# Performance work log

Measured on AMD Instinct MI355X. Metric: run time of the kernel, lower is better.

The kernel has to match this reference:

```python
import jax, jax.numpy as jnp
import numpy as np

B, T, D, H = 512, 128, 384, 6
DH = D // H  # 64
DFF = 4 * D  # 1536
EPS = 1e-5


def layer_norm(x, g, b):
    mu = jnp.mean(x, axis=-1, keepdims=True)
    var = jnp.var(x, axis=-1, keepdims=True)
    return (x - mu) * jax.lax.rsqrt(var + EPS) * g + b


def setup_inputs() -> dict:
    key = jax.random.key(0)
    ks = jax.random.split(key, 12)
    s = lambda *sh: 1.0 / np.sqrt(sh[0])
    return {
        "x": jax.random.normal(ks[0], (B, T, D), dtype=jnp.float32),
        "Wq": jax.random.normal(ks[1], (D, D), dtype=jnp.float32) * s(D),
        "Wk": jax.random.normal(ks[2], (D, D), dtype=jnp.float32) * s(D),
        "Wv": jax.random.normal(ks[3], (D, D), dtype=jnp.float32) * s(D),
        "Wo": jax.random.normal(ks[4], (D, D), dtype=jnp.float32) * s(D),
        "bo": jnp.zeros((D,), jnp.float32),
        "W1": jax.random.normal(ks[5], (D, DFF), dtype=jnp.float32) * s(D),
        "b1": jnp.zeros((DFF,), jnp.float32),
        "W2": jax.random.normal(ks[6], (DFF, D), dtype=jnp.float32) * s(DFF),
        "b2": jnp.zeros((D,), jnp.float32),
        "g1": jnp.ones((D,), jnp.float32),
        "be1": jnp.zeros((D,), jnp.float32),
        "g2": jnp.ones((D,), jnp.float32),
        "be2": jnp.zeros((D,), jnp.float32),
    }


def reference(x, Wq, Wk, Wv, Wo, bo, W1, b1, W2, b2, g1, be1, g2, be2):
    # --- multi-head causal self-attention on layer_norm1(x) ---
    h = layer_norm(x, g1, be1)
    q = (h @ Wq).reshape(B, T, H, DH)
    k = (h @ Wk).reshape(B, T, H, DH)
    v = (h @ Wv).reshape(B, T, H, DH)
    scores = jnp.einsum("bthd,bshd->bhts", q, k) * (DH ** -0.5)  # [B,H,T,T]
    causal = jnp.tril(jnp.ones((T, T), dtype=bool))
    scores = jnp.where(causal, scores, -jnp.inf)
    attn = jax.nn.softmax(scores, axis=-1)
    o = jnp.einsum("bhts,bshd->bthd", attn, v).reshape(B, T, D)
    x = x + o @ Wo + bo
    # --- feed-forward on layer_norm2(x) ---
    h2 = layer_norm(x, g2, be2)
    ff = jax.nn.relu(h2 @ W1 + b1) @ W2 + b2
    return x + ff
```

## Files before the change

kernel.cpp:

```cpp
#include <hip/hip_runtime.h>

#define B_   512
#define T_   128
#define D_   384
#define H_   6
#define DH_  64
#define DFF_ 1536
#define NROW (B_*T_)

typedef __attribute__((ext_vector_type(8))) short bf16x8;
typedef __attribute__((ext_vector_type(4))) float f32x4;

__device__ __forceinline__ unsigned short f2bf(float f) {
  union { float f; unsigned u; } v; v.f = f;
  unsigned r = v.u + 0x7fffu + ((v.u >> 16) & 1u);
  return (unsigned short)(r >> 16);
}

#define GLDS16(gp, lp)                                                     \
  __builtin_amdgcn_global_load_lds(                                        \
      (const __attribute__((address_space(1))) void*)(gp),                 \
      (__attribute__((address_space(3))) void*)(lp), 16, 0, 0)

#define BAR_LGKM() asm volatile("s_waitcnt lgkmcnt(0)\n\ts_barrier" ::: "memory")

__global__ void wt_kernel(const float* __restrict__ W, unsigned short* __restrict__ WT,
                          int K, int Nn) {
  int id = blockIdx.x * 256 + threadIdx.x;
  if (id >= K * Nn) return;
  int n = id % Nn, kk = id / Nn;
  WT[(size_t)n * K + kk] = f2bf(W[(size_t)kk * Nn + n]);
}

__global__ void pack_w1(const unsigned short* __restrict__ W1T,
                        unsigned short* __restrict__ W1P) {
  int tid = blockIdx.x * 256 + threadIdx.x;
  int lane = tid & 63, frag = tid >> 6;
  int k = frag % 12, t2 = frag / 12;
  int mi = t2 & 1, t3 = t2 >> 1;
  int w = t3 & 3, c = t3 >> 2;
  int l15 = lane & 15, lq = lane >> 4;
  int r = c * 128 + w * 32 + mi * 16 + l15;
  int col = k * 32 + lq * 8;
  *(int4*)(W1P + (size_t)tid * 8) = *(const int4*)(W1T + (size_t)r * 384 + col);
}
__global__ void pack_w2(const unsigned short* __restrict__ W2T,
                        unsigned short* __restrict__ W2P) {
  int tid = blockIdx.x * 256 + threadIdx.x;
  int lane = tid & 63, frag = tid >> 6;
  int kk = frag & 3, t2 = frag >> 2;
  int c = t2 % 12, t3 = t2 / 12;
  int mi = t3 % 6, w = t3 / 6;
  int l15 = lane & 15, lq = lane >> 4;
  int r = w * 96 + mi * 16 + l15;
  int col = c * 128 + kk * 32 + lq * 8;
  *(int4*)(W2P + (size_t)tid * 8) = *(const int4*)(W2T + (size_t)r * 1536 + col);
}

__global__ __launch_bounds__(256) void ln_kernel(const float* __restrict__ x,
                                                 const float* __restrict__ g,
                                                 const float* __restrict__ be,
                                                 unsigned short* __restrict__ out) {
  int row = (blockIdx.x * 256 + threadIdx.x) >> 6;
  int l = threadIdx.x & 63;
  const float* xr = x + (size_t)row * D_;
  float v[6]; float s = 0.f, ss = 0.f;
  #pragma unroll
  for (int i = 0; i < 6; ++i) { v[i] = xr[l + i*64]; s += v[i]; ss += v[i]*v[i]; }
  #pragma unroll
  for (int m = 1; m < 64; m <<= 1) { s += __shfl_xor(s, m); ss += __shfl_xor(ss, m); }
  float mu  = s * (1.f / D_);
  float var = ss * (1.f / D_) - mu * mu;
  float rs  = rsqrtf(var + 1e-5f);
  unsigned short* orow = out + (size_t)row * D_;
  #pragma unroll
  for (int i = 0; i < 6; ++i) {
    int c = l + i*64;
    orow[c] = f2bf((v[i] - mu) * rs * g[c] + be[c]);
  }
}

template<int EPI>
__global__ __launch_bounds__(256) void gemm_bt(const unsigned short* __restrict__ A,
                                               const unsigned short* __restrict__ BT,
                                               void* __restrict__ Cc,
                                               const float* __restrict__ bias,
                                               const float* __restrict__ res,
                                               int Nn, int K) {
  __shared__ unsigned short As[2][128][32];
  __shared__ unsigned short Bs[2][128][32];
  int tid = threadIdx.x, w = tid >> 6, l = tid & 63;
  int wr = w >> 1, wc = w & 1;

  int ncol = gridDim.y;
  int nwg  = gridDim.x * ncol;
  int lin  = blockIdx.y * gridDim.x + blockIdx.x;
  int cpx  = nwg >> 3;
  int swz  = (lin & 7) * cpx + (lin >> 3);
  size_t R0 = (size_t)(swz / ncol) * 128;
  int C0 = (swz % ncol) * 128;

  int seg0 = (w * 2 + 0) * 16;
  int seg1 = (w * 2 + 1) * 16;
  int srow0 = seg0 + (l >> 2);
  int srow1 = seg1 + (l >> 2);
  int scol  = (l & 3) * 8;

  const unsigned short* ga0 = A  + (R0 + srow0) * K + scol;
  const unsigned short* ga1 = A  + (R0 + srow1) * K + scol;
  const unsigned short* gb0 = BT + (size_t)(C0 + srow0) * K + scol;
  const unsigned short* gb1 = BT + (size_t)(C0 + srow1) * K + scol;

  f32x4 acc[4][4];
  #pragma unroll
  for (int i = 0; i < 4; ++i)
    #pragma unroll
    for (int j = 0; j < 4; ++j) acc[i][j] = (f32x4){0.f, 0.f, 0.f, 0.f};

  GLDS16(ga0, &As[0][seg0][0]);
  GLDS16(ga1, &As[0][seg1][0]);
  GLDS16(gb0, &Bs[0][seg0][0]);
  GLDS16(gb1, &Bs[0][seg1][0]);
  ga0 += 32; ga1 += 32; gb0 += 32; gb1 += 32;

  int nk = K >> 5;
  for (int t = 0; t < nk; ++t) {
    int cur = t & 1;
    __syncthreads();
    if (t + 1 < nk) {
      GLDS16(ga0, &As[cur ^ 1][seg0][0]);
      GLDS16(ga1, &As[cur ^ 1][seg1][0]);
      GLDS16(gb0, &Bs[cur ^ 1][seg0][0]);
      GLDS16(gb1, &Bs[cur ^ 1][seg1][0]);
      ga0 += 32; ga1 += 32; gb0 += 32; gb1 += 32;
    }
    bf16x8 af[4], bf[4];
    #pragma unroll
    for (int mi = 0; mi < 4; ++mi)
      af[mi] = *(const bf16x8*)(&As[cur][wr*64 + mi*16 + (l & 15)][(l >> 4) * 8]);
    #pragma unroll
    for (int ni = 0; ni < 4; ++ni)
      bf[ni] = *(const bf16x8*)(&Bs[cur][wc*64 + ni*16 + (l & 15)][(l >> 4) * 8]);
    #pragma unroll
    for (int mi = 0; mi < 4; ++mi)
      #pragma unroll
      for (int ni = 0; ni < 4; ++ni)
        acc[mi][ni] = __builtin_amdgcn_mfma_f32_16x16x32_bf16(af[mi], bf[ni], acc[mi][ni], 0, 0, 0);
  }

  #pragma unroll
  for (int mi = 0; mi < 4; ++mi) {
    #pragma unroll
    for (int ni = 0; ni < 4; ++ni) {
      int col = C0 + wc*64 + ni*16 + (l & 15);
      #pragma unroll
      for (int j = 0; j < 4; ++j) {
        size_t row = R0 + wr*64 + mi*16 + ((l >> 4) << 2) + j;
        float vv = acc[mi][ni][j];
        if (EPI == 1) {
          ((float*)Cc)[row * Nn + col] = vv + bias[col] + res[row * Nn + col];
        } else {
          int buf = col / 384, c2 = col - buf * 384;
          ((unsigned short*)Cc)[(size_t)buf * NROW * 384 + row * 384 + c2] = f2bf(vv);
        }
      }
    }
  }
}

#define LDA3(dst, pA, k0)                                                    \
  { _Pragma("unroll") for (int kq = 0; kq < 3; ++kq)                         \
      dst[kq] = *(const bf16x8*)((pA) + ((k0) + kq) * 512); }

#define CMP3(buf, k0, acc)                                                   \
  { _Pragma("unroll") for (int kq = 0; kq < 3; ++kq) {                       \
      bf16x8 bfr[4];                                                         \
      _Pragma("unroll") for (int ni = 0; ni < 4; ++ni)                       \
        bfr[ni] = *(const bf16x8*)(smem + (ni*12 + (k0)+kq)*1024 + l*16);    \
      _Pragma("unroll") for (int ni = 0; ni < 4; ++ni)                       \
        acc[ni] = __builtin_amdgcn_mfma_f32_16x16x32_bf16(                   \
            buf[kq], bfr[ni], acc[ni], 0, 0, 0);                             \
    } }

__global__ __launch_bounds__(512, 4) void ffn_fused(
    const unsigned short* __restrict__ h2,
    const unsigned short* __restrict__ w1P,
    const unsigned short* __restrict__ w2P,
    const float* __restrict__ b1,
    const float* __restrict__ b2,
    float* __restrict__ out)
{
  __shared__ __align__(16) char smem[65536];
  int tid = threadIdx.x, w = tid >> 6, l = tid & 63;
  int l15 = l & 15, lq = l >> 4;
  size_t R0 = (size_t)blockIdx.x * 64;

  {
    int row = tid >> 3, gi = row >> 4, l15w = row & 15;
    int cbase = (tid & 7) * 48;
    const unsigned short* src = h2 + (R0 + row) * 384 + cbase;
    #pragma unroll
    for (int i = 0; i < 6; ++i) {
      int col = cbase + i * 8;
      int k = col >> 5, lqw = (col >> 3) & 3;
      *(int4*)(smem + (gi*12 + k)*1024 + (lqw*16 + l15w)*16) = *(const int4*)(src + i*8);
    }
  }
  __syncthreads();

  f32x4 oacc[3][4];
  #pragma unroll
  for (int i = 0; i < 3; ++i)
    #pragma unroll
    for (int j = 0; j < 4; ++j) oacc[i][j] = (f32x4){0.f, 0.f, 0.f, 0.f};

  const unsigned short* w1b = w1P + w * 6144  + l * 8;
  const unsigned short* w2b = w2P + w * 73728 + l * 8;

  #define LDV(dst, pV, kk)                                                   \
    { _Pragma("unroll") for (int mi = 0; mi < 3; ++mi)                       \
        dst[mi] = *(const bf16x8*)((pV) + mi * 24576 + (kk) * 512); }

  #define CMPV(buf, kk)                                                      \
    { bf16x8 bv[4];                                                          \
      _Pragma("unroll") for (int ni = 0; ni < 4; ++ni)                       \
        bv[ni] = *(const bf16x8*)(smem + 49152 + (ni*4 + (kk))*1024 + l*16); \
      _Pragma("unroll") for (int mi = 0; mi < 3; ++mi)                       \
        _Pragma("unroll") for (int ni = 0; ni < 4; ++ni)                     \
          oacc[mi][ni] = __builtin_amdgcn_mfma_f32_16x16x32_bf16(            \
              buf[mi], bv[ni], oacc[mi][ni], 0, 0, 0);                       \
    }

  bf16x8 afA[3], afB[3];
  bf16x8 avA[3], avB[3];

  LDA3(afA, w1b, 0)

  for (int c = 0; c < 12; ++c) {
    const unsigned short* pA = w1b + (size_t)c * 49152;
    const unsigned short* pV = w2b + c * 2048;

    f32x4 pacc[4];
    #pragma unroll
    for (int j = 0; j < 4; ++j) pacc[j] = (f32x4){0.f, 0.f, 0.f, 0.f};

    LDA3(afB, pA, 3)
    __builtin_amdgcn_s_setprio(1); CMP3(afA, 0, pacc) __builtin_amdgcn_s_setprio(0);
    LDA3(afA, pA, 6)
    __builtin_amdgcn_s_setprio(1); CMP3(afB, 3, pacc) __builtin_amdgcn_s_setprio(0);
    LDA3(afB, pA, 9)
    __builtin_amdgcn_s_setprio(1); CMP3(afA, 6, pacc) __builtin_amdgcn_s_setprio(0);
    LDV(avA, pV, 0)
    __builtin_amdgcn_s_setprio(1); CMP3(afB, 9, pacc) __builtin_amdgcn_s_setprio(0);

    {
      int fcb = c * 128 + w * 16 + lq * 4;
      float4 bb = *(const float4*)(b1 + fcb);
      unsigned pw = (unsigned)(49152 + (w >> 1) * 1024 +
                    (((w & 1) * 2 + (lq >> 1)) * 16 + l15) * 16 + (lq & 1) * 8);
      #pragma unroll
      for (int ni = 0; ni < 4; ++ni) {
        float p0 = pacc[ni][0] + bb.x;
        float p1 = pacc[ni][1] + bb.y;
        float p2 = pacc[ni][2] + bb.z;
        float p3 = pacc[ni][3] + bb.w;
        ushort4 pk;
        pk.x = f2bf(p0 > 0.f ? p0 : 0.f);
        pk.y = f2bf(p1 > 0.f ? p1 : 0.f);
        pk.z = f2bf(p2 > 0.f ? p2 : 0.f);
        pk.w = f2bf(p3 > 0.f ? p3 : 0.f);
        *(ushort4*)(smem + pw + ni * 4096) = pk;
      }
    }
    BAR_LGKM();

    const unsigned short* pAn = w1b + (size_t)(c < 11 ? c + 1 : 11) * 49152;
    LDV(avB, pV, 1)
    __builtin_amdgcn_s_setprio(1); CMPV(avA, 0) __builtin_amdgcn_s_setprio(0);
    LDV(avA, pV, 2)
    __builtin_amdgcn_s_setprio(1); CMPV(avB, 1) __builtin_amdgcn_s_setprio(0);
    LDV(avB, pV, 3)
    __builtin_amdgcn_s_setprio(1); CMPV(avA, 2) __builtin_amdgcn_s_setprio(0);
    LDA3(afA, pAn, 0)
    __builtin_amdgcn_s_setprio(1); CMPV(avB, 3) __builtin_amdgcn_s_setprio(0);
    BAR_LGKM();
  }
  #undef LDV
  #undef CMPV

  #pragma unroll
  for (int mi = 0; mi < 3; ++mi) {
    int ocb = w * 48 + mi * 16 + lq * 4;
    float4 b2v = *(const float4*)(b2 + ocb);
    #pragma unroll
    for (int ni = 0; ni < 4; ++ni) {
      size_t row = R0 + ni * 16 + l15;
      float* op = out + row * D_ + ocb;
      float4 r = *(const float4*)op;
      float4 o;
      o.x = oacc[mi][ni][0] + b2v.x + r.x;
      o.y = oacc[mi][ni][1] + b2v.y + r.y;
      o.z = oacc[mi][ni][2] + b2v.z + r.z;
      o.w = oacc[mi][ni][3] + b2v.w + r.w;
      *(float4*)op = o;
    }
  }
}

__global__ __launch_bounds__(256) void attn_kernel(const unsigned short* __restrict__ q,
                                                   const unsigned short* __restrict__ k,
                                                   const unsigned short* __restrict__ v,
                                                   unsigned short* __restrict__ o) {
  __shared__ __align__(16) char smem[52224];
  unsigned short (*Ks)[72]       = (unsigned short(*)[72])smem;
  unsigned short (*Ps)[32][136]  = (unsigned short(*)[32][136])smem;
  unsigned short (*Vt)[136]      = (unsigned short(*)[136])(smem + 34816);

  int bh = blockIdx.x;
  int b = bh / H_, h = bh % H_;
  int tid = threadIdx.x, w = tid >> 6, l = tid & 63;

  const unsigned short* kb = k + ((size_t)b * T_) * D_ + h * DH_;
  const unsigned short* vb = v + ((size_t)b * T_) * D_ + h * DH_;
  #pragma unroll
  for (int it = 0; it < 4; ++it) {
    int id = it * 256 + tid;
    int s = id >> 3, c8 = (id & 7) * 8;
    int4 kv = *(const int4*)(kb + (size_t)s * D_ + c8);
    *(int4*)(&Ks[s][c8]) = kv;
    int4 vv = *(const int4*)(vb + (size_t)s * D_ + c8);
    const unsigned short* pe = (const unsigned short*)&vv;
    #pragma unroll
    for (int j2 = 0; j2 < 8; ++j2) Vt[c8 + j2][s] = pe[j2];
  }
  __syncthreads();

  const unsigned short* qbp = q + ((size_t)b * T_) * D_ + h * DH_;
  int rowbase = w * 32;
  bf16x8 aq[2][2];
  #pragma unroll
  for (int mi = 0; mi < 2; ++mi)
    #pragma unroll
    for (int ks = 0; ks < 2; ++ks)
      aq[mi][ks] = *(const bf16x8*)(qbp + (size_t)(rowbase + mi*16 + (l & 15)) * D_
                                        + ks*32 + ((l >> 4) << 3));

  f32x4 accs[2][8];
  #pragma unroll
  for (int i = 0; i < 2; ++i)
    #pragma unroll
    for (int j = 0; j < 8; ++j) accs[i][j] = (f32x4){0.f, 0.f, 0.f, 0.f};
  #pragma unroll
  for (int ks = 0; ks < 2; ++ks) {
    bf16x8 bk[8];
    #pragma unroll
    for (int ni = 0; ni < 8; ++ni)
      bk[ni] = *(const bf16x8*)(&Ks[ni*16 + (l & 15)][ks*32 + ((l >> 4) << 3)]);
    __builtin_amdgcn_s_setprio(1);
    #pragma unroll
    for (int mi = 0; mi < 2; ++mi)
      #pragma unroll
      for (int ni = 0; ni < 8; ++ni)
        accs[mi][ni] = __builtin_amdgcn_mfma_f32_16x16x32_bf16(aq[mi][ks], bk[ni], accs[mi][ni], 0, 0, 0);
    __builtin_amdgcn_s_setprio(0);
  }
  __syncthreads();

  #pragma unroll
  for (int mi = 0; mi < 2; ++mi) {
    #pragma unroll
    for (int j = 0; j < 4; ++j) {
      int t = rowbase + mi*16 + ((l >> 4) << 2) + j;
      float mx = -1e30f;
      #pragma unroll
      for (int ni = 0; ni < 8; ++ni) {
        int scol = ni*16 + (l & 15);
        float sv = accs[mi][ni][j] * 0.125f;
        sv = (scol <= t) ? sv : -1e30f;
        accs[mi][ni][j] = sv;
        mx = fmaxf(mx, sv);
      }
      mx = fmaxf(mx, __shfl_xor(mx, 1));
      mx = fmaxf(mx, __shfl_xor(mx, 2));
      mx = fmaxf(mx, __shfl_xor(mx, 4));
      mx = fmaxf(mx, __shfl_xor(mx, 8));
      float sum = 0.f;
      #pragma unroll
      for (int ni = 0; ni < 8; ++ni) {
        float e = __expf(accs[mi][ni][j] - mx);
        accs[mi][ni][j] = e;
        sum += e;
      }
      sum += __shfl_xor(sum, 1);
      sum += __shfl_xor(sum, 2);
      sum += __shfl_xor(sum, 4);
      sum += __shfl_xor(sum, 8);
      float inv = 1.f / sum;
      #pragma unroll
      for (int ni = 0; ni < 8; ++ni)
        Ps[w][mi*16 + ((l >> 4) << 2) + j][ni*16 + (l & 15)] = f2bf(accs[mi][ni][j] * inv);
    }
  }
  __syncthreads();

  f32x4 acco[2][4];
  #pragma unroll
  for (int i = 0; i < 2; ++i)
    #pragma unroll
    for (int j = 0; j < 4; ++j) acco[i][j] = (f32x4){0.f, 0.f, 0.f, 0.f};
  #pragma unroll
  for (int ks = 0; ks < 4; ++ks) {
    bf16x8 ap[2], bv[4];
    #pragma unroll
    for (int mi = 0; mi < 2; ++mi)
      ap[mi] = *(const bf16x8*)(&Ps[w][mi*16 + (l & 15)][ks*32 + ((l >> 4) << 3)]);
    #pragma unroll
    for (int ni = 0; ni < 4; ++ni)
      bv[ni] = *(const bf16x8*)(&Vt[ni*16 + (l & 15)][ks*32 + ((l >> 4) << 3)]);
    __builtin_amdgcn_s_setprio(1);
    #pragma unroll
    for (int mi = 0; mi < 2; ++mi)
      #pragma unroll
      for (int ni = 0; ni < 4; ++ni)
        acco[mi][ni] = __builtin_amdgcn_mfma_f32_16x16x32_bf16(ap[mi], bv[ni], acco[mi][ni], 0, 0, 0);
    __builtin_amdgcn_s_setprio(0);
  }

  unsigned short* ob = o + ((size_t)b * T_) * D_ + h * DH_;
  #pragma unroll
  for (int mi = 0; mi < 2; ++mi)
    #pragma unroll
    for (int ni = 0; ni < 4; ++ni)
      #pragma unroll
      for (int j = 0; j < 4; ++j) {
        int t = rowbase + mi*16 + ((l >> 4) << 2) + j;
        int d = ni*16 + (l & 15);
        ob[(size_t)t * D_ + d] = f2bf(acco[mi][ni][j]);
      }
}

extern "C" void kernel_launch(void* const* d_in, const int* in_sizes, int n_in,
                              void* d_out, int out_size, void* d_ws, size_t ws_size,
                              hipStream_t stream) {
  const float* x   = (const float*)d_in[0];
  const float* Wq  = (const float*)d_in[1];
  const float* Wk  = (const float*)d_in[2];
  const float* Wv  = (const float*)d_in[3];
  const float* Wo  = (const float*)d_in[4];
  const float* bo  = (const float*)d_in[5];
  const float* W1  = (const float*)d_in[6];
  const float* b1  = (const float*)d_in[7];
  const float* W2  = (const float*)d_in[8];
  const float* b2  = (const float*)d_in[9];
  const float* g1  = (const float*)d_in[10];
  const float* be1 = (const float*)d_in[11];
  const float* g2  = (const float*)d_in[12];
  const float* be2 = (const float*)d_in[13];

  char* ws = (char*)d_ws;
  unsigned short* hb   = (unsigned short*)(ws);
  unsigned short* qb   = (unsigned short*)(ws +  50331648);
  unsigned short* kbuf = (unsigned short*)(ws + 100663296);
  unsigned short* vbuf = (unsigned short*)(ws + 150994944);
  unsigned short* wqT  = (unsigned short*)(ws + 201326592);
  unsigned short* wkT  = wqT + 147456;
  unsigned short* wvT  = wkT + 147456;
  unsigned short* woT  = wvT + 147456;
  unsigned short* w1T  = woT + 147456;
  unsigned short* w2T  = w1T + 589824;
  unsigned short* w1P  = w2T + 589824;
  unsigned short* w2P  = w1P + 589824;
  float* x2 = (float*)d_out;
  (void)kbuf; (void)vbuf;

  wt_kernel<<<dim3(576),  256, 0, stream>>>(Wq, wqT, 384, 384);
  wt_kernel<<<dim3(576),  256, 0, stream>>>(Wk, wkT, 384, 384);
  wt_kernel<<<dim3(576),  256, 0, stream>>>(Wv, wvT, 384, 384);
  wt_kernel<<<dim3(576),  256, 0, stream>>>(Wo, woT, 384, 384);
  wt_kernel<<<dim3(2304), 256, 0, stream>>>(W1, w1T, 384, 1536);
  wt_kernel<<<dim3(2304), 256, 0, stream>>>(W2, w2T, 1536, 384);
  pack_w1<<<dim3(288), 256, 0, stream>>>(w1T, w1P);
  pack_w2<<<dim3(288), 256, 0, stream>>>(w2T, w2P);

  ln_kernel<<<dim3(NROW / 4), 256, 0, stream>>>(x, g1, be1, hb);

  gemm_bt<3><<<dim3(NROW / 128, 9), 256, 0, stream>>>(hb, wqT, qb, nullptr, nullptr, 1152, 384);

  attn_kernel<<<dim3(B_ * H_), 256, 0, stream>>>(qb, kbuf, vbuf, qb);

  gemm_bt<1><<<dim3(NROW / 128, 3), 256, 0, stream>>>(qb, woT, x2, bo, x, 384, 384);

  ln_kernel<<<dim3(NROW / 4), 256, 0, stream>>>((const float*)x2, g2, be2, hb);

  ffn_fused<<<dim3(NROW / 64), 512, 0, stream>>>(hb, w1P, w2P, b1, b2, x2);
}
```

Before: 447.1 us.

## Replace QKV projection GEMM with dedicated kernel streaming prepacked weights from global

Adds a specialized QKV GEMM kernel. Each 512-thread block stages a 32-row tile of the layernormed activations in LDS once, streams prepacked Wqkv fragments directly from global memory into registers with software prefetch and setprio around the MFMAs, and writes bf16 outputs through LDS as coalesced 16-byte stores. The Wq/Wk/Wv transposes are made contiguous and packed by the existing pack_w1 kernel, and the generic gemm_bt loses its bf16 scatter epilogue. This aims to remove the strided 2-byte scatter stores and the LDS staging of B tiles. In exchange every block re-reads the full weight matrix, which relies on cache hits, and each tile covers only 32 rows.

```diff
diff --git a/kernel.cpp b/kernel.cpp
--- a/kernel.cpp
+++ b/kernel.cpp
@@ -80,6 +80,95 @@
   }
 }
 
+__global__ __launch_bounds__(512, 4) void qkv_gemm(
+    const unsigned short* __restrict__ h, const unsigned short* __restrict__ wP,
+    unsigned short* __restrict__ qkv)
+{
+  __shared__ __align__(16) char smem[25600];
+  int tid = threadIdx.x, w = tid >> 6, l = tid & 63;
+  int l15 = l & 15, lq = l >> 4;
+  size_t R0 = (size_t)blockIdx.x * 32;
+
+  {
+    int row = tid >> 4, gi = row >> 4, l15w = row & 15;
+    const unsigned short* src = h + (R0 + row) * 384 + (tid & 15) * 24;
+    #pragma unroll
+    for (int i = 0; i < 3; ++i) {
+      int col = (tid & 15) * 24 + i * 8;
+      int k = col >> 5, lqw = (col >> 3) & 3;
+      *(int4*)(smem + (gi*12 + k)*1024 + (lqw*16 + l15w)*16) = *(const int4*)(src + i*8);
+    }
+  }
+  __syncthreads();
+
+  f32x4 acc[9][2];
+  #pragma unroll
+  for (int c = 0; c < 9; ++c)
+    #pragma unroll
+    for (int ni = 0; ni < 2; ++ni) acc[c][ni] = (f32x4){0.f, 0.f, 0.f, 0.f};
+
+  const unsigned short* wb = wP + l * 8;
+
+  #define LDG(dst, cb, k)                                                    \
+    { _Pragma("unroll") for (int ci = 0; ci < 3; ++ci)                       \
+        dst[ci] = *(const bf16x8*)(wb + (((cb)+ci)*8 + w) * 6144 + (k) * 512); }
+
+  #define CMPG(buf, cb)                                                      \
+    { _Pragma("unroll") for (int ci = 0; ci < 3; ++ci)                       \
+        _Pragma("unroll") for (int ni = 0; ni < 2; ++ni)                     \
+          acc[(cb)+ci][ni] = __builtin_amdgcn_mfma_f32_16x16x32_bf16(        \
+              buf[ci], bfr[ni], acc[(cb)+ci][ni], 0, 0, 0); }
+
+  bf16x8 a0[3], a1[3], a2[3];
+  LDG(a0, 0, 0)
+
+  for (int k = 0; k < 12; ++k) {
+    bf16x8 bfr[2];
+    #pragma unroll
+    for (int ni = 0; ni < 2; ++ni)
+      bfr[ni] = *(const bf16x8*)(smem + (ni*12 + k)*1024 + l*16);
+    int kn = (k < 11) ? k + 1 : 11;
+    LDG(a1, 3, k)
+    __builtin_amdgcn_s_setprio(1); CMPG(a0, 0) __builtin_amdgcn_s_setprio(0);
+    LDG(a2, 6, k)
+    __builtin_amdgcn_s_setprio(1); CMPG(a1, 3) __builtin_amdgcn_s_setprio(0);
+    LDG(a0, 0, kn)
+    __builtin_amdgcn_s_setprio(1); CMPG(a2, 6) __builtin_amdgcn_s_setprio(0);
+  }
+  #undef LDG
+  #undef CMPG
+
+  __syncthreads();
+  #pragma unroll
+  for (int buf = 0; buf < 3; ++buf) {
+    #pragma unroll
+    for (int ci = 0; ci < 3; ++ci) {
+      int c = buf * 3 + ci;
+      #pragma unroll
+      for (int ni = 0; ni < 2; ++ni) {
+        int row = ni * 16 + l15;
+        ushort4 pk;
+        pk.x = f2bf(acc[c][ni][0]);
+        pk.y = f2bf(acc[c][ni][1]);
+        pk.z = f2bf(acc[c][ni][2]);
+        pk.w = f2bf(acc[c][ni][3]);
+        *(ushort4*)(smem + row * 784 + ci * 256 + w * 32 + lq * 8) = pk;
+      }
+    }
+    __syncthreads();
+    {
+      int row = tid >> 4;
+      unsigned short* obase = qkv + (size_t)buf * NROW * 384 + (R0 + row) * 384;
+      #pragma unroll
+      for (int i = 0; i < 3; ++i) {
+        int ob = (tid & 15) * 16 + i * 256;
+        *(int4*)(obase + (ob >> 1)) = *(const int4*)(smem + row * 784 + ob);
+      }
+    }
+    __syncthreads();
+  }
+}
+
 template<int EPI>
 __global__ __launch_bounds__(256) void gemm_bt(const unsigned short* __restrict__ A,
                                                const unsigned short* __restrict__ BT,
@@ -157,12 +246,7 @@
       for (int j = 0; j < 4; ++j) {
         size_t row = R0 + wr*64 + mi*16 + ((l >> 4) << 2) + j;
         float vv = acc[mi][ni][j];
-        if (EPI == 1) {
-          ((float*)Cc)[row * Nn + col] = vv + bias[col] + res[row * Nn + col];
-        } else {
-          int buf = col / 384, c2 = col - buf * 384;
-          ((unsigned short*)Cc)[(size_t)buf * NROW * 384 + row * 384 + c2] = f2bf(vv);
-        }
+        ((float*)Cc)[row * Nn + col] = vv + bias[col] + res[row * Nn + col];
       }
     }
   }
@@ -458,33 +542,33 @@
   const float* be2 = (const float*)d_in[13];
 
   char* ws = (char*)d_ws;
-  unsigned short* hb   = (unsigned short*)(ws);
-  unsigned short* qb   = (unsigned short*)(ws +  50331648);
-  unsigned short* kbuf = (unsigned short*)(ws + 100663296);
-  unsigned short* vbuf = (unsigned short*)(ws + 150994944);
-  unsigned short* wqT  = (unsigned short*)(ws + 201326592);
-  unsigned short* wkT  = wqT + 147456;
-  unsigned short* wvT  = wkT + 147456;
-  unsigned short* woT  = wvT + 147456;
-  unsigned short* w1T  = woT + 147456;
-  unsigned short* w2T  = w1T + 589824;
-  unsigned short* w1P  = w2T + 589824;
-  unsigned short* w2P  = w1P + 589824;
+  unsigned short* hb    = (unsigned short*)(ws);
+  unsigned short* qb    = (unsigned short*)(ws +  50331648);
+  unsigned short* kbuf  = (unsigned short*)(ws + 100663296);
+  unsigned short* vbuf  = (unsigned short*)(ws + 150994944);
+  unsigned short* wqT   = (unsigned short*)(ws + 201326592);
+  unsigned short* woT   = wqT + 442368;
+  unsigned short* w1T   = woT + 147456;
+  unsigned short* w2T   = w1T + 589824;
+  unsigned short* w1P   = w2T + 589824;
+  unsigned short* w2P   = w1P + 589824;
+  unsigned short* wqkvP = w2P + 589824;
   float* x2 = (float*)d_out;
   (void)kbuf; (void)vbuf;
 
-  wt_kernel<<<dim3(576),  256, 0, stream>>>(Wq, wqT, 384, 384);
-  wt_kernel<<<dim3(576),  256, 0, stream>>>(Wk, wkT, 384, 384);
-  wt_kernel<<<dim3(576),  256, 0, stream>>>(Wv, wvT, 384, 384);
-  wt_kernel<<<dim3(576),  256, 0, stream>>>(Wo, woT, 384, 384);
+  wt_kernel<<<dim3(576),  256, 0, stream>>>(Wq, wqT,          384, 384);
+  wt_kernel<<<dim3(576),  256, 0, stream>>>(Wk, wqT + 147456, 384, 384);
+  wt_kernel<<<dim3(576),  256, 0, stream>>>(Wv, wqT + 294912, 384, 384);
+  wt_kernel<<<dim3(576),  256, 0, stream>>>(Wo, woT,          384, 384);
   wt_kernel<<<dim3(2304), 256, 0, stream>>>(W1, w1T, 384, 1536);
   wt_kernel<<<dim3(2304), 256, 0, stream>>>(W2, w2T, 1536, 384);
+  pack_w1<<<dim3(216), 256, 0, stream>>>(wqT, wqkvP);
   pack_w1<<<dim3(288), 256, 0, stream>>>(w1T, w1P);
   pack_w2<<<dim3(288), 256, 0, stream>>>(w2T, w2P);
 
   ln_kernel<<<dim3(NROW / 4), 256, 0, stream>>>(x, g1, be1, hb);
 
-  gemm_bt<3><<<dim3(NROW / 128, 9), 256, 0, stream>>>(hb, wqT, qb, nullptr, nullptr, 1152, 384);
+  qkv_gemm<<<dim3(NROW / 32), 512, 0, stream>>>(hb, wqkvP, qb);
 
   attn_kernel<<<dim3(B_ * H_), 256, 0, stream>>>(qb, kbuf, vbuf, qb);
 
```

Measured after the change: 442.2 us. No clear change (-1.1%).
